# Performance work log

Hardware: AMD Instinct MI355X
Metric: run time of the kernel (lower is better)

Reference implementation:

```python
import jax, jax.numpy as jnp
import numpy as np

L = 2048      # sequence length (self.len)
DIM = 1024    # model dim
DPOS = 128    # positional encoding dim
B = 4
EPS = 1e-5


def make_pe(length, d):
    # standard sinusoidal positional encoding, shape [length, d]
    pos = np.arange(length)[:, None].astype(np.float32)
    div = np.exp(-np.arange(0, d, 2).astype(np.float32) * (np.log(10000.0) / d))
    pe = np.zeros((length, d), dtype=np.float32)
    pe[:, 0::2] = np.sin(pos * div)
    pe[:, 1::2] = np.cos(pos * div)
    return jnp.asarray(pe)


def setup_inputs() -> dict:
    key = jax.random.key(0)
    ks = jax.random.split(key, 16)
    s = lambda fan_in: 1.0 / np.sqrt(fan_in)
    inp = {
        "z": jax.random.normal(ks[0], (B, L, DIM), jnp.float32),
        "x": jax.random.normal(ks[1], (B, L, DIM), jnp.float32),
        "a": jax.random.normal(ks[2], (1,), jnp.float32),
        "pe": make_pe(L, DPOS),
        # torch Linear weights stored [out, in]
        "w_pos1": jax.random.normal(ks[3], (DPOS + DIM, DPOS), jnp.float32) * s(DPOS),
        "b_pos1": jnp.zeros((DPOS + DIM,), jnp.float32),
        "w_pos2": jax.random.normal(ks[4], (DIM, DPOS + DIM), jnp.float32) * s(DPOS + DIM),
        "b_pos2": jnp.zeros((DIM,), jnp.float32),
        "w1": jax.random.normal(ks[5], (DIM * 2, DIM), jnp.float32) * s(DIM),
        "b1": jnp.zeros((DIM * 2,), jnp.float32),
        "w2": jax.random.normal(ks[6], (DIM, DIM * 2), jnp.float32) * s(DIM * 2),
        "b2": jnp.zeros((DIM,), jnp.float32),
        "w3": jax.random.normal(ks[7], (DIM * 2, DIM), jnp.float32) * s(DIM),
        "b3": jnp.zeros((DIM * 2,), jnp.float32),
        "w4": jax.random.normal(ks[8], (DIM, DIM * 2), jnp.float32) * s(DIM * 2),
        "b4": jnp.zeros((DIM,), jnp.float32),
        "ln_g": jnp.ones((DIM,), jnp.float32),
        "ln_b": jnp.zeros((DIM,), jnp.float32),
    }
    return inp


def _layer_norm(v, g, b):
    mu = jnp.mean(v, axis=-1, keepdims=True)
    var = jnp.var(v, axis=-1, keepdims=True)
    return (v - mu) * jax.lax.rsqrt(var + EPS) * g + b


def _lin(v, w, b):
    return v @ w.T + b


def reference(z, x, a, pe, w_pos1, b_pos1, w_pos2, b_pos2,
              w1, b1, w2, b2, w3, b3, w4, b4, ln_g, ln_b):
    zn = _layer_norm(z, ln_g, ln_b)                       # [B, L, D]
    fz = jnp.fft.rfft(zn, n=2 * L, axis=1)                # [B, L+1, D] complex
    expa = jnp.exp(a)                                     # [1]
    window = jnp.exp(-jnp.arange(L, dtype=jnp.float32) * expa)  # [L]
    h = _lin(pe, w_pos1, b_pos1)                          # [L, DPOS+D]
    h = jax.nn.gelu(h, approximate=False)
    h = _lin(h, w_pos2, b_pos2)                           # [L, D] (dropout eval = id)
    wfh = jnp.fft.rfft(window[:, None] * h, n=2 * L, axis=0)  # [L+1, D]
    cwhz = jnp.fft.irfft(wfh * fz, axis=1)[:, :L, :]      # [B, L, D]
    x1 = _lin(x, w1, b1)
    x1 = jax.nn.gelu(x1, approximate=False)
    x1 = _lin(x1, w2, b2)
    x1 = x1 * cwhz + z
    y = _layer_norm(x1, ln_g, ln_b)
    y = _lin(y, w3, b3)
    y = jax.nn.gelu(y, approximate=False)
    y = _lin(y, w4, b4)
    return y + x1
```

## Files before the change

### kernel.cpp

```cpp
#include <hip/hip_runtime.h>
#include <hip/hip_bf16.h>
#include <cmath>

typedef __hip_bfloat16 bf16;
typedef __attribute__((ext_vector_type(8))) short bf16x8;
typedef __attribute__((ext_vector_type(4))) float f32x4;

static __device__ __forceinline__ float b2f(bf16 v) { return __bfloat162float(v); }
static __device__ __forceinline__ bf16 f2b(float v) { return __float2bfloat16(v); }
static __device__ __forceinline__ float us2f(unsigned short u) {
  return __uint_as_float(((unsigned)u) << 16);
}

static __device__ __forceinline__ void gl2lds16(const bf16* g, bf16* l) {
  __builtin_amdgcn_global_load_lds(
      (const __attribute__((address_space(1))) void*)g,
      (__attribute__((address_space(3))) void*)l, 16, 0, 0);
}

static __device__ __forceinline__ float gelu_fast(float v) {
  float u = v * (0.7978845608f + 0.0356774081f * v * v);
  float e = __expf(2.f * u);
  return v * (e * __frcp_rn(e + 1.f));
}

static __device__ __forceinline__ int xcd_swz(int lid, int nwg) {
  const int q = nwg >> 3, r = nwg & 7;
  const int xcd = lid & 7, loc = lid >> 3;
  const int base = (xcd < r) ? xcd * (q + 1) : r * (q + 1) + (xcd - r) * q;
  return base + loc;
}

struct CvtSegs { const float* src[7]; int blk_off[8]; };
__global__ __launch_bounds__(256) void cvt7_k(CvtSegs s, bf16* __restrict__ dst0)
{
  int b = blockIdx.x;
  int seg = 0;
#pragma unroll
  for (int i = 0; i < 6; ++i) seg += (b >= s.blk_off[i + 1]) ? 1 : 0;
  const float* src = s.src[seg] + (size_t)(b - s.blk_off[seg]) * 1024;
  bf16* dst = dst0 + (size_t)b * 1024;
  int idx = threadIdx.x * 4;
  float4 v = *(const float4*)(src + idx);
  union { bf16 bb[4]; ushort4 u; } o;
  o.bb[0] = f2b(v.x); o.bb[1] = f2b(v.y); o.bb[2] = f2b(v.z); o.bb[3] = f2b(v.w);
  *(ushort4*)(dst + idx) = o.u;
}

__global__ __launch_bounds__(256) void cvt_k(const float* __restrict__ in,
                                             bf16* __restrict__ out, int n)
{
  int idx = (blockIdx.x * 256 + threadIdx.x) * 4;
  if (idx >= n) return;
  float4 v = *(const float4*)(in + idx);
  union { bf16 b[4]; ushort4 u; } o;
  o.b[0] = f2b(v.x); o.b[1] = f2b(v.y); o.b[2] = f2b(v.z); o.b[3] = f2b(v.w);
  *(ushort4*)(out + idx) = o.u;
}

__global__ __launch_bounds__(256) void ln_k(const float* __restrict__ X, bf16* __restrict__ Y,
                                            const float* __restrict__ gamma,
                                            const float* __restrict__ beta)
{
  __shared__ float red[16];
  const int row = blockIdx.x, tid = threadIdx.x;
  float4 v = *(const float4*)(X + (size_t)row * 1024 + tid * 4);
  float s  = v.x + v.y + v.z + v.w;
  float s2 = v.x * v.x + v.y * v.y + v.z * v.z + v.w * v.w;
#pragma unroll
  for (int m = 32; m; m >>= 1) { s += __shfl_xor(s, m, 64); s2 += __shfl_xor(s2, m, 64); }
  const int wid = tid >> 6;
  if ((tid & 63) == 0) { red[wid] = s; red[wid + 8] = s2; }
  __syncthreads();
  s  = red[0] + red[1] + red[2] + red[3];
  s2 = red[8] + red[9] + red[10] + red[11];
  const float mu  = s * (1.f / 1024.f);
  const float var = s2 * (1.f / 1024.f) - mu * mu;
  const float rs  = rsqrtf(var + 1e-5f);
  float4 g = *(const float4*)(gamma + tid * 4);
  float4 bt = *(const float4*)(beta + tid * 4);
  union { bf16 b[4]; ushort4 u; } o;
  o.b[0] = f2b((v.x - mu) * rs * g.x + bt.x);
  o.b[1] = f2b((v.y - mu) * rs * g.y + bt.y);
  o.b[2] = f2b((v.z - mu) * rs * g.z + bt.z);
  o.b[3] = f2b((v.w - mu) * rs * g.w + bt.w);
  *(ushort4*)(Y + (size_t)row * 1024 + tid * 4) = o.u;
}

template<int EPI, int QCLIP = 0>
__global__ __launch_bounds__(256, 3) void gemm_k(
    const bf16* __restrict__ A, const bf16* __restrict__ W,
    const float* __restrict__ bias, void* __restrict__ Out,
    const void* __restrict__ aux0, const void* __restrict__ aux1,
    int M, int N, int K)
{
  __shared__ bf16 As[3][128 * 32];
  __shared__ bf16 Bs[3][128 * 32];
  const int tid = threadIdx.x;
  const int wid = tid >> 6, lane = tid & 63;
  const int quad = lane >> 4, l16 = lane & 15;
  const int wm = wid >> 1, wn = wid & 1;

  const int nwg = gridDim.x * gridDim.y;
  int lid = xcd_swz(blockIdx.y * gridDim.x + blockIdx.x, nwg);
  const int bx = lid % gridDim.x, by = lid / gridDim.x;
  const int m0 = by * 128, n0 = bx * 128;

  if (QCLIP > 0) {
    const float smax = 20.7f / __expf(((const float*)aux1)[0]);
    if ((float)(m0 - QCLIP) > smax) return;
  }

  f32x4 acc[4][4];
#pragma unroll
  for (int i = 0; i < 4; ++i)
#pragma unroll
    for (int j = 0; j < 4; ++j) acc[i][j] = (f32x4){0.f, 0.f, 0.f, 0.f};

  const bf16 *ga[2], *gb[2];
  int ldso[2];
#pragma unroll
  for (int r = 0; r < 2; ++r) {
    int p = r * 256 + wid * 64 + lane;
    int row = p >> 2;
    int sko = ((p & 3) ^ ((p >> 3) & 3)) << 3;
    ga[r] = A + (size_t)(m0 + row) * K + sko;
    gb[r] = W + (size_t)(n0 + row) * K + sko;
    ldso[r] = (r * 256 + wid * 64) * 8;
  }
  int apos[4], bpos[4];
#pragma unroll
  for (int i = 0; i < 4; ++i) {
    int ar = wm * 64 + i * 16 + l16;
    apos[i] = (ar * 4 + (quad ^ ((ar >> 1) & 3))) * 8;
    int br = wn * 64 + i * 16 + l16;
    bpos[i] = (br * 4 + (quad ^ ((br >> 1) & 3))) * 8;
  }

  const int niter = K >> 5;
#pragma unroll
  for (int t = 0; t < 2; ++t)
#pragma unroll
    for (int r = 0; r < 2; ++r) {
      gl2lds16(ga[r] + t * 32, &As[t][ldso[r]]);
      gl2lds16(gb[r] + t * 32, &Bs[t][ldso[r]]);
    }

  int cur = 0;
  for (int k = 0; k < niter; ++k) {
    if (k == niter - 1) { asm volatile("s_waitcnt vmcnt(0)" ::: "memory"); }
    else               { asm volatile("s_waitcnt vmcnt(4)" ::: "memory"); }
    asm volatile("s_barrier" ::: "memory");

    const bf16* as = As[cur];
    const bf16* bs = Bs[cur];
    bf16x8 af[4], bfr[4];
#pragma unroll
    for (int i = 0; i < 4; ++i) af[i]  = *(const bf16x8*)(as + apos[i]);
#pragma unroll
    for (int j = 0; j < 4; ++j) bfr[j] = *(const bf16x8*)(bs + bpos[j]);
    asm volatile("s_waitcnt lgkmcnt(0)" ::: "memory");

    if (k + 2 < niter) {
      int nb = cur + 2; if (nb >= 3) nb -= 3;
#pragma unroll
      for (int r = 0; r < 2; ++r) {
        gl2lds16(ga[r] + (k + 2) * 32, &As[nb][ldso[r]]);
        gl2lds16(gb[r] + (k + 2) * 32, &Bs[nb][ldso[r]]);
      }
    }
#pragma unroll
    for (int i = 0; i < 4; ++i)
#pragma unroll
      for (int j = 0; j < 4; ++j)
        acc[i][j] = __builtin_amdgcn_mfma_f32_16x16x32_bf16(af[i], bfr[j], acc[i][j], 0, 0, 0);
    cur += 1; if (cur == 3) cur = 0;
  }

  float expa = 0.f;
  if (EPI == 1) expa = expf(((const float*)aux0)[0]);
#pragma unroll
  for (int i = 0; i < 4; ++i) {
    const int gm_base = m0 + wm * 64 + i * 16 + quad * 4;
#pragma unroll
    for (int j = 0; j < 4; ++j) {
      const int gn = n0 + wn * 64 + j * 16 + l16;
      const float bv = bias[gn];
#pragma unroll
      for (int r = 0; r < 4; ++r) {
        const int gm = gm_base + r;
        const size_t off = (size_t)gm * N + gn;
        float v = acc[i][j][r] + bv;
        if (EPI == 0) ((bf16*)Out)[off] = f2b(gelu_fast(v));
        else if (EPI == 1) ((float*)Out)[off] = v * expf(-(float)gm * expa);
        else if (EPI == 2) ((float*)Out)[off] = v * ((const float*)aux0)[off] + ((const float*)aux1)[off];
        else ((float*)Out)[off] = v + ((const float*)aux0)[off];
      }
    }
  }
}

template<int EPI, int QCLIP = 0>
__global__ __launch_bounds__(256, 2) void gemmw_k(
    const bf16* __restrict__ A, const bf16* __restrict__ W,
    const float* __restrict__ bias, void* __restrict__ Out,
    const void* __restrict__ aux0, const void* __restrict__ aux1,
    int M, int N, int K)
{
  __shared__ bf16 As[2][128 * 64];
  __shared__ bf16 Bs[2][128 * 64];
  const int tid = threadIdx.x;
  const int wid = tid >> 6, lane = tid & 63;
  const int quad = lane >> 4, l16 = lane & 15;
  const int wm = wid >> 1, wn = wid & 1;

  const int nwg = gridDim.x * gridDim.y;
  int lid = xcd_swz(blockIdx.y * gridDim.x + blockIdx.x, nwg);
  const int bx = lid % gridDim.x, by = lid / gridDim.x;
  const int m0 = by * 128, n0 = bx * 128;

  if (QCLIP > 0) {
    const float smax = 20.7f / __expf(((const float*)aux0)[0]);
    if ((float)(m0 - QCLIP) > smax) return;
  }

  f32x4 acc[4][4];
#pragma unroll
  for (int i = 0; i < 4; ++i)
#pragma unroll
    for (int j = 0; j < 4; ++j) acc[i][j] = (f32x4){0.f, 0.f, 0.f, 0.f};

  const bf16 *ga[4], *gb[4];
  int ldso[4];
#pragma unroll
  for (int r = 0; r < 4; ++r) {
    int p = r * 256 + tid;
    int row = p >> 3;
    int c = (p & 7) ^ (row & 7);
    ga[r] = A + (size_t)(m0 + row) * K + c * 8;
    gb[r] = W + (size_t)(n0 + row) * K + c * 8;
    ldso[r] = p * 8;
  }
  int apos[4][2], bpos[4][2];
#pragma unroll
  for (int i = 0; i < 4; ++i) {
    int ar = wm * 64 + i * 16 + l16;
    int br = wn * 64 + i * 16 + l16;
#pragma unroll
    for (int ks = 0; ks < 2; ++ks) {
      apos[i][ks] = ar * 64 + (((quad + 4 * ks) ^ (ar & 7)) * 8);
      bpos[i][ks] = br * 64 + (((quad + 4 * ks) ^ (br & 7)) * 8);
    }
  }

  const int niter = K >> 6;

#pragma unroll
  for (int r = 0; r < 4; ++r) {
    gl2lds16(ga[r], &As[0][ldso[r]]);
    gl2lds16(gb[r], &Bs[0][ldso[r]]);
  }

  for (int k = 0; k < niter; ++k) {
    asm volatile("s_waitcnt vmcnt(0)" ::: "memory");
    asm volatile("s_barrier" ::: "memory");
    const int cur = k & 1;
    if (k + 1 < niter) {
      const int nxt = cur ^ 1;
#pragma unroll
      for (int r = 0; r < 4; ++r) {
        gl2lds16(ga[r] + (k + 1) * 64, &As[nxt][ldso[r]]);
        gl2lds16(gb[r] + (k + 1) * 64, &Bs[nxt][ldso[r]]);
      }
    }
    const bf16* as = As[cur];
    const bf16* bs = Bs[cur];
    bf16x8 af[4][2], bfr[4][2];
#pragma unroll
    for (int i = 0; i < 4; ++i)
#pragma unroll
      for (int ks = 0; ks < 2; ++ks) af[i][ks] = *(const bf16x8*)(as + apos[i][ks]);
#pragma unroll
    for (int j = 0; j < 4; ++j)
#pragma unroll
      for (int ks = 0; ks < 2; ++ks) bfr[j][ks] = *(const bf16x8*)(bs + bpos[j][ks]);
    asm volatile("s_waitcnt lgkmcnt(0)" ::: "memory");

#pragma unroll
    for (int ks = 0; ks < 2; ++ks)
#pragma unroll
      for (int i = 0; i < 4; ++i)
#pragma unroll
        for (int j = 0; j < 4; ++j)
          acc[i][j] = __builtin_amdgcn_mfma_f32_16x16x32_bf16(af[i][ks], bfr[j][ks], acc[i][j], 0, 0, 0);
  }

  float expa = 0.f;
  if (EPI == 1) expa = expf(((const float*)aux0)[0]);
#pragma unroll
  for (int i = 0; i < 4; ++i) {
    const int gm_base = m0 + wm * 64 + i * 16 + quad * 4;
#pragma unroll
    for (int j = 0; j < 4; ++j) {
      const int gn = n0 + wn * 64 + j * 16 + l16;
      const float bv = bias[gn];
#pragma unroll
      for (int r = 0; r < 4; ++r) {
        const int gm = gm_base + r;
        const size_t off = (size_t)gm * N + gn;
        float v = acc[i][j][r] + bv;
        if (EPI == 0) ((bf16*)Out)[off] = f2b(gelu_fast(v));
        else if (EPI == 1) ((float*)Out)[off] = v * expf(-(float)gm * expa);
        else if (EPI == 2) ((float*)Out)[off] = v * ((const float*)aux0)[off] + ((const float*)aux1)[off];
        else ((float*)Out)[off] = v + ((const float*)aux0)[off];
      }
    }
  }
}

__global__ __launch_bounds__(256) void conv_k(
    const bf16* __restrict__ zn,
    const float* __restrict__ wh,
    const float* __restrict__ a,
    float* __restrict__ out)
{
  __shared__ float whs[64 * 64];
  __shared__ float znt[128 * 64];
  const int tid = threadIdx.x;
  const int dd = tid & 63, ttg = tid >> 6;
  const int t0 = blockIdx.x * 64, d0 = blockIdx.y * 64, b = blockIdx.z;
  const float expa = expf(a[0]);
  const float smax = 20.7f / expa;
  const unsigned short* znu = (const unsigned short*)zn;

  float acc[16];
#pragma unroll
  for (int q = 0; q < 16; ++q) acc[q] = 0.f;

  for (int sb = 0; sb <= t0 + 63; sb += 64) {
    if ((float)sb > smax) break;
    float4 wv4[4];
#pragma unroll
    for (int i = 0; i < 4; ++i) {
      int cc = tid + 256 * i;
      int row = cc >> 4, dq = (cc & 15) * 4;
      wv4[i] = *(const float4*)&wh[(size_t)(sb + row) * 1024 + d0 + dq];
    }
    ushort4 zv4[8];
#pragma unroll
    for (int i = 0; i < 8; ++i) {
      int cc = tid + 256 * i;
      int row = cc >> 4, dq = (cc & 15) * 4;
      int u = t0 - sb - 64 + row;
      zv4[i] = (u >= 0) ? *(const ushort4*)&znu[((size_t)b * 2048 + u) * 1024 + d0 + dq]
                        : make_ushort4(0, 0, 0, 0);
    }
#pragma unroll
    for (int i = 0; i < 4; ++i) {
      int cc = tid + 256 * i;
      *(float4*)&whs[(cc >> 4) * 64 + (cc & 15) * 4] = wv4[i];
    }
#pragma unroll
    for (int i = 0; i < 8; ++i) {
      int cc = tid + 256 * i;
      float4 o;
      o.x = us2f(zv4[i].x); o.y = us2f(zv4[i].y); o.z = us2f(zv4[i].z); o.w = us2f(zv4[i].w);
      *(float4*)&znt[(cc >> 4) * 64 + (cc & 15) * 4] = o;
    }
    __syncthreads();

    float win[16];
#pragma unroll
    for (int q = 0; q < 16; ++q) win[q] = znt[(ttg * 16 + q + 64) * 64 + dd];
#pragma unroll
    for (int ss = 0; ss < 64; ++ss) {
      float wv = whs[ss * 64 + dd];
#pragma unroll
      for (int q = 0; q < 16; ++q) acc[q] += wv * win[q];
      if (ss < 63) {
#pragma unroll
        for (int q = 15; q >= 1; --q) win[q] = win[q - 1];
        win[0] = znt[(ttg * 16 + 63 - ss) * 64 + dd];
      }
    }
    __syncthreads();
  }
#pragma unroll
  for (int q = 0; q < 16; ++q) {
    int t = t0 + ttg * 16 + q;
    out[((size_t)b * 2048 + t) * 1024 + d0 + dd] = acc[q];
  }
}

extern "C" void kernel_launch(void* const* d_in, const int* in_sizes, int n_in,
                              void* d_out, int out_size, void* d_ws, size_t ws_size,
                              hipStream_t stream)
{
  const float* z      = (const float*)d_in[0];
  const float* x      = (const float*)d_in[1];
  const float* a      = (const float*)d_in[2];
  const float* pe     = (const float*)d_in[3];
  const float* w_pos1 = (const float*)d_in[4];
  const float* b_pos1 = (const float*)d_in[5];
  const float* w_pos2 = (const float*)d_in[6];
  const float* b_pos2 = (const float*)d_in[7];
  const float* w1     = (const float*)d_in[8];
  const float* b1     = (const float*)d_in[9];
  const float* w2     = (const float*)d_in[10];
  const float* b2     = (const float*)d_in[11];
  const float* w3     = (const float*)d_in[12];
  const float* b3     = (const float*)d_in[13];
  const float* w4     = (const float*)d_in[14];
  const float* b4     = (const float*)d_in[15];
  const float* ln_g   = (const float*)d_in[16];
  const float* ln_b   = (const float*)d_in[17];

  char* ws = (char*)d_ws;
  bf16* pe_bf  = (bf16*)(ws + 0);
  bf16* wp1_bf = (bf16*)(ws + 524288);
  bf16* wp2_bf = (bf16*)(ws + 819200);
  bf16* w1_bf  = (bf16*)(ws + 3178496);
  bf16* w2_bf  = (bf16*)(ws + 7372800);
  bf16* w3_bf  = (bf16*)(ws + 11567104);
  bf16* w4_bf  = (bf16*)(ws + 15761408);
  bf16* h1     = (bf16*)(ws + 19955712);
  bf16* zn_bf  = (bf16*)(ws + 24674304);
  bf16* x_bf   = (bf16*)(ws + 41451520);
  float* wh    = (float*)(ws + 58228736);
  float* cwhz  = (float*)(ws + 66617344);
  bf16*  x1n   = (bf16*)(ws + 66617344);
  bf16*  g     = (bf16*)(ws + 100171776);
  float* x1    = (float*)(ws + 24674304);
  float* out   = (float*)d_out;

  CvtSegs segs;
  segs.src[0] = pe;  segs.src[1] = w_pos1; segs.src[2] = w_pos2;
  segs.src[3] = w1;  segs.src[4] = w2;     segs.src[5] = w3; segs.src[6] = w4;
  int bo[8] = {0, 256, 400, 1552, 3600, 5648, 7696, 9744};
  for (int i = 0; i < 8; ++i) segs.blk_off[i] = bo[i];
  cvt7_k<<<9744, 256, 0, stream>>>(segs, (bf16*)ws);
  cvt_k<<<8192, 256, 0, stream>>>(x, x_bf, 8388608);

  ln_k<<<8192, 256, 0, stream>>>(z, zn_bf, ln_g, ln_b);
  gemm_k<0, 190><<<dim3(9, 16), 256, 0, stream>>>(pe_bf, wp1_bf, b_pos1, h1, nullptr, a, 2048, 1152, 128);
  gemmw_k<1, 63><<<dim3(8, 16), 256, 0, stream>>>(h1, wp2_bf, b_pos2, wh, a, nullptr, 2048, 1024, 1152);
  conv_k<<<dim3(32, 16, 4), 256, 0, stream>>>(zn_bf, wh, a, cwhz);
  gemm_k<0><<<dim3(16, 64), 256, 0, stream>>>(x_bf, w1_bf, b1, g, nullptr, nullptr, 8192, 2048, 1024);
  gemmw_k<2><<<dim3(8, 64), 256, 0, stream>>>(g, w2_bf, b2, x1, cwhz, z, 8192, 1024, 2048);
  ln_k<<<8192, 256, 0, stream>>>(x1, x1n, ln_g, ln_b);
  gemm_k<0><<<dim3(16, 64), 256, 0, stream>>>(x1n, w3_bf, b3, g, nullptr, nullptr, 8192, 2048, 1024);
  gemmw_k<3><<<dim3(8, 64), 256, 0, stream>>>(g, w4_bf, b4, out, x1, nullptr, 8192, 1024, 2048);
}
```

Measured before the change: 422.6 us.

## Merge prep kernels and batch pos-MLP GEMM1 with x GEMM1

Folds the weight conversion, x conversion and z layernorm into one prep launch. Adds a new GEMM kernel that runs the x@w1 GEMM and the positional pe@w_pos1 GEMM in one grid, using a 3-stage, 32-wide K pipeline. The conv inner loop uses circular register indexing instead of shifting the window array. This cuts launch count and lets the small GEMM fill idle CUs, but depends on the new pipeline matching the old GEMM's efficiency.

```diff
diff --git a/kernel.cpp b/kernel.cpp
--- a/kernel.cpp
+++ b/kernel.cpp
@@ -32,30 +32,55 @@
 }
 
 struct CvtSegs { const float* src[7]; int blk_off[8]; };
-__global__ __launch_bounds__(256) void cvt7_k(CvtSegs s, bf16* __restrict__ dst0)
-{
-  int b = blockIdx.x;
-  int seg = 0;
-#pragma unroll
-  for (int i = 0; i < 6; ++i) seg += (b >= s.blk_off[i + 1]) ? 1 : 0;
-  const float* src = s.src[seg] + (size_t)(b - s.blk_off[seg]) * 1024;
-  bf16* dst = dst0 + (size_t)b * 1024;
-  int idx = threadIdx.x * 4;
-  float4 v = *(const float4*)(src + idx);
-  union { bf16 bb[4]; ushort4 u; } o;
-  o.bb[0] = f2b(v.x); o.bb[1] = f2b(v.y); o.bb[2] = f2b(v.z); o.bb[3] = f2b(v.w);
-  *(ushort4*)(dst + idx) = o.u;
-}
-
-__global__ __launch_bounds__(256) void cvt_k(const float* __restrict__ in,
-                                             bf16* __restrict__ out, int n)
-{
-  int idx = (blockIdx.x * 256 + threadIdx.x) * 4;
-  if (idx >= n) return;
-  float4 v = *(const float4*)(in + idx);
-  union { bf16 b[4]; ushort4 u; } o;
-  o.b[0] = f2b(v.x); o.b[1] = f2b(v.y); o.b[2] = f2b(v.z); o.b[3] = f2b(v.w);
-  *(ushort4*)(out + idx) = o.u;
+__global__ __launch_bounds__(256) void prep_k(
+    CvtSegs s, bf16* __restrict__ dst0,
+    const float* __restrict__ x, bf16* __restrict__ x_bf,
+    const float* __restrict__ z, bf16* __restrict__ zn,
+    const float* __restrict__ gamma, const float* __restrict__ beta)
+{
+  const int b = blockIdx.x, tid = threadIdx.x;
+  if (b < 9744) {
+    int seg = 0;
+#pragma unroll
+    for (int i = 0; i < 6; ++i) seg += (b >= s.blk_off[i + 1]) ? 1 : 0;
+    const float* src = s.src[seg] + (size_t)(b - s.blk_off[seg]) * 1024;
+    bf16* dst = dst0 + (size_t)b * 1024;
+    int idx = tid * 4;
+    float4 v = *(const float4*)(src + idx);
+    union { bf16 bb[4]; ushort4 u; } o;
+    o.bb[0] = f2b(v.x); o.bb[1] = f2b(v.y); o.bb[2] = f2b(v.z); o.bb[3] = f2b(v.w);
+    *(ushort4*)(dst + idx) = o.u;
+  } else if (b < 17936) {
+    size_t idx = ((size_t)(b - 9744) * 256 + tid) * 4;
+    float4 v = *(const float4*)(x + idx);
+    union { bf16 bb[4]; ushort4 u; } o;
+    o.bb[0] = f2b(v.x); o.bb[1] = f2b(v.y); o.bb[2] = f2b(v.z); o.bb[3] = f2b(v.w);
+    *(ushort4*)(x_bf + idx) = o.u;
+  } else {
+    __shared__ float red[16];
+    const int row = b - 17936;
+    float4 v = *(const float4*)(z + (size_t)row * 1024 + tid * 4);
+    float sa  = v.x + v.y + v.z + v.w;
+    float s2 = v.x * v.x + v.y * v.y + v.z * v.z + v.w * v.w;
+#pragma unroll
+    for (int m = 32; m; m >>= 1) { sa += __shfl_xor(sa, m, 64); s2 += __shfl_xor(s2, m, 64); }
+    const int wid = tid >> 6;
+    if ((tid & 63) == 0) { red[wid] = sa; red[wid + 8] = s2; }
+    __syncthreads();
+    sa = red[0] + red[1] + red[2] + red[3];
+    s2 = red[8] + red[9] + red[10] + red[11];
+    const float mu  = sa * (1.f / 1024.f);
+    const float var = s2 * (1.f / 1024.f) - mu * mu;
+    const float rs  = rsqrtf(var + 1e-5f);
+    float4 g = *(const float4*)(gamma + tid * 4);
+    float4 bt = *(const float4*)(beta + tid * 4);
+    union { bf16 bb[4]; ushort4 u; } o;
+    o.bb[0] = f2b((v.x - mu) * rs * g.x + bt.x);
+    o.bb[1] = f2b((v.y - mu) * rs * g.y + bt.y);
+    o.bb[2] = f2b((v.z - mu) * rs * g.z + bt.z);
+    o.bb[3] = f2b((v.w - mu) * rs * g.w + bt.w);
+    *(ushort4*)(zn + (size_t)row * 1024 + tid * 4) = o.u;
+  }
 }
 
 __global__ __launch_bounds__(256) void ln_k(const float* __restrict__ X, bf16* __restrict__ Y,
@@ -200,6 +225,118 @@
   }
 }
 
+__global__ __launch_bounds__(256, 3) void gemm52_k(
+    const bf16* __restrict__ A5, const bf16* __restrict__ W5,
+    const float* __restrict__ b5, bf16* __restrict__ O5,
+    const bf16* __restrict__ A2, const bf16* __restrict__ W2,
+    const float* __restrict__ b2, bf16* __restrict__ O2,
+    const float* __restrict__ a)
+{
+  __shared__ bf16 As[3][128 * 32];
+  __shared__ bf16 Bs[3][128 * 32];
+  const int tid = threadIdx.x;
+  const int wid = tid >> 6, lane = tid & 63;
+  const int quad = lane >> 4, l16 = lane & 15;
+  const int wm = wid >> 1, wn = wid & 1;
+
+  const bf16 *A, *W;
+  const float* bias;
+  bf16* Out;
+  int N, K, m0, n0;
+  if (blockIdx.x < 1024) {
+    int lid = xcd_swz(blockIdx.x, 1024);
+    m0 = (lid / 16) * 128; n0 = (lid % 16) * 128;
+    A = A5; W = W5; bias = b5; Out = O5; N = 2048; K = 1024;
+  } else {
+    int lid = xcd_swz(blockIdx.x - 1024, 144);
+    m0 = (lid / 9) * 128; n0 = (lid % 9) * 128;
+    A = A2; W = W2; bias = b2; Out = O2; N = 1152; K = 128;
+    const float smax = 20.7f / __expf(a[0]);
+    if ((float)(m0 - 190) > smax) return;
+  }
+
+  f32x4 acc[4][4];
+#pragma unroll
+  for (int i = 0; i < 4; ++i)
+#pragma unroll
+    for (int j = 0; j < 4; ++j) acc[i][j] = (f32x4){0.f, 0.f, 0.f, 0.f};
+
+  const bf16 *ga[2], *gb[2];
+  int ldso[2];
+#pragma unroll
+  for (int r = 0; r < 2; ++r) {
+    int p = r * 256 + wid * 64 + lane;
+    int row = p >> 2;
+    int sko = ((p & 3) ^ ((p >> 3) & 3)) << 3;
+    ga[r] = A + (size_t)(m0 + row) * K + sko;
+    gb[r] = W + (size_t)(n0 + row) * K + sko;
+    ldso[r] = (r * 256 + wid * 64) * 8;
+  }
+  int apos[4], bpos[4];
+#pragma unroll
+  for (int i = 0; i < 4; ++i) {
+    int ar = wm * 64 + i * 16 + l16;
+    apos[i] = (ar * 4 + (quad ^ ((ar >> 1) & 3))) * 8;
+    int br = wn * 64 + i * 16 + l16;
+    bpos[i] = (br * 4 + (quad ^ ((br >> 1) & 3))) * 8;
+  }
+
+  const int niter = K >> 5;
+#pragma unroll
+  for (int t = 0; t < 2; ++t)
+#pragma unroll
+    for (int r = 0; r < 2; ++r) {
+      gl2lds16(ga[r] + t * 32, &As[t][ldso[r]]);
+      gl2lds16(gb[r] + t * 32, &Bs[t][ldso[r]]);
+    }
+
+  int cur = 0;
+  for (int k = 0; k < niter; ++k) {
+    if (k == niter - 1) { asm volatile("s_waitcnt vmcnt(0)" ::: "memory"); }
+    else               { asm volatile("s_waitcnt vmcnt(4)" ::: "memory"); }
+    asm volatile("s_barrier" ::: "memory");
+
+    const bf16* as = As[cur];
+    const bf16* bs = Bs[cur];
+    bf16x8 af[4], bfr[4];
+#pragma unroll
+    for (int i = 0; i < 4; ++i) af[i]  = *(const bf16x8*)(as + apos[i]);
+#pragma unroll
+    for (int j = 0; j < 4; ++j) bfr[j] = *(const bf16x8*)(bs + bpos[j]);
+    asm volatile("s_waitcnt lgkmcnt(0)" ::: "memory");
+
+    if (k + 2 < niter) {
+      int nb = cur + 2; if (nb >= 3) nb -= 3;
+#pragma unroll
+      for (int r = 0; r < 2; ++r) {
+        gl2lds16(ga[r] + (k + 2) * 32, &As[nb][ldso[r]]);
+        gl2lds16(gb[r] + (k + 2) * 32, &Bs[nb][ldso[r]]);
+      }
+    }
+#pragma unroll
+    for (int i = 0; i < 4; ++i)
+#pragma unroll
+      for (int j = 0; j < 4; ++j)
+        acc[i][j] = __builtin_amdgcn_mfma_f32_16x16x32_bf16(af[i], bfr[j], acc[i][j], 0, 0, 0);
+    cur += 1; if (cur == 3) cur = 0;
+  }
+
+#pragma unroll
+  for (int i = 0; i < 4; ++i) {
+    const int gm_base = m0 + wm * 64 + i * 16 + quad * 4;
+#pragma unroll
+    for (int j = 0; j < 4; ++j) {
+      const int gn = n0 + wn * 64 + j * 16 + l16;
+      const float bv = bias[gn];
+#pragma unroll
+      for (int r = 0; r < 4; ++r) {
+        const size_t off = (size_t)(gm_base + r) * N + gn;
+        Out[off] = f2b(gelu_fast(acc[i][j][r] + bv));
+      }
+    }
+  }
+}
+
 template<int EPI, int QCLIP = 0>
 __global__ __launch_bounds__(256, 2) void gemmw_k(
     const bf16* __restrict__ A, const bf16* __restrict__ W,
@@ -371,17 +508,13 @@
 
     float win[16];
 #pragma unroll
-    for (int q = 0; q < 16; ++q) win[q] = znt[(ttg * 16 + q + 64) * 64 + dd];
+    for (int r = 0; r < 16; ++r) win[r] = znt[(ttg * 16 + r + 64) * 64 + dd];
 #pragma unroll
     for (int ss = 0; ss < 64; ++ss) {
       float wv = whs[ss * 64 + dd];
 #pragma unroll
-      for (int q = 0; q < 16; ++q) acc[q] += wv * win[q];
-      if (ss < 63) {
-#pragma unroll
-        for (int q = 15; q >= 1; --q) win[q] = win[q - 1];
-        win[0] = znt[(ttg * 16 + 63 - ss) * 64 + dd];
-      }
+      for (int q = 0; q < 16; ++q) acc[q] += wv * win[(q - ss) & 15];
+      if (ss < 63) win[(15 - ss) & 15] = znt[(ttg * 16 + 63 - ss) * 64 + dd];
     }
     __syncthreads();
   }
@@ -438,14 +571,11 @@
   segs.src[3] = w1;  segs.src[4] = w2;     segs.src[5] = w3; segs.src[6] = w4;
   int bo[8] = {0, 256, 400, 1552, 3600, 5648, 7696, 9744};
   for (int i = 0; i < 8; ++i) segs.blk_off[i] = bo[i];
-  cvt7_k<<<9744, 256, 0, stream>>>(segs, (bf16*)ws);
-  cvt_k<<<8192, 256, 0, stream>>>(x, x_bf, 8388608);
-
-  ln_k<<<8192, 256, 0, stream>>>(z, zn_bf, ln_g, ln_b);
-  gemm_k<0, 190><<<dim3(9, 16), 256, 0, stream>>>(pe_bf, wp1_bf, b_pos1, h1, nullptr, a, 2048, 1152, 128);
+
+  prep_k<<<26128, 256, 0, stream>>>(segs, (bf16*)ws, x, x_bf, z, zn_bf, ln_g, ln_b);
+  gemm52_k<<<1168, 256, 0, stream>>>(x_bf, w1_bf, b1, g, pe_bf, wp1_bf, b_pos1, h1, a);
   gemmw_k<1, 63><<<dim3(8, 16), 256, 0, stream>>>(h1, wp2_bf, b_pos2, wh, a, nullptr, 2048, 1024, 1152);
   conv_k<<<dim3(32, 16, 4), 256, 0, stream>>>(zn_bf, wh, a, cwhz);
-  gemm_k<0><<<dim3(16, 64), 256, 0, stream>>>(x_bf, w1_bf, b1, g, nullptr, nullptr, 8192, 2048, 1024);
   gemmw_k<2><<<dim3(8, 64), 256, 0, stream>>>(g, w2_bf, b2, x1, cwhz, z, 8192, 1024, 2048);
   ln_k<<<8192, 256, 0, stream>>>(x1, x1n, ln_g, ln_b);
   gemm_k<0><<<dim3(16, 64), 256, 0, stream>>>(x1n, w3_bf, b3, g, nullptr, nullptr, 8192, 2048, 1024);
```

After: 414.3 us. 1.02x faster.
